# Kernel optimization log

Hardware: AMD Instinct MI355X
Metric: run time of the kernel (lower is better)

The kernel has to match this reference:

```python
import jax, jax.numpy as jnp
import numpy as np

N, E, G = 100000, 1600000, 64   # nodes, edges, graphs
IN, H, OUT = 32, 128, 3


def setup_inputs() -> dict:
    key = jax.random.key(0)
    ks = jax.random.split(key, 24)
    def w(k, i, o):
        return (jax.random.normal(k, (i, o), jnp.float32) / np.sqrt(i)).astype(jnp.float32)
    inp = {
        "x": jax.random.normal(ks[0], (N, IN), jnp.float32),
        "edge_index": jax.random.randint(ks[1], (2, E), 0, N, dtype=jnp.int32).astype(jnp.int64),
        "batch": jnp.sort(jax.random.randint(ks[2], (N,), 0, G, dtype=jnp.int32)).astype(jnp.int64),
        # SAGEConv layer 0 (in->hidden): lin_l (neighbors, with bias), lin_r (root, no bias)
        "Wl0": w(ks[3], IN, H), "bl0": jnp.zeros((H,), jnp.float32), "Wr0": w(ks[4], IN, H),
        # SAGEConv layers 1,2 (hidden->hidden)
        "Wl1": w(ks[5], H, H), "bl1": jnp.zeros((H,), jnp.float32), "Wr1": w(ks[6], H, H),
        "Wl2": w(ks[7], H, H), "bl2": jnp.zeros((H,), jnp.float32), "Wr2": w(ks[8], H, H),
        # output head
        "Wfc": w(ks[9], H, OUT), "bfc": jnp.zeros((OUT,), jnp.float32),
        # aux MLP on (dim1, dim3)
        "Wa1": w(ks[10], 2, H), "ba1": jnp.zeros((H,), jnp.float32),
        "Wa2": w(ks[11], H, H), "ba2": jnp.zeros((H,), jnp.float32),
        "Wao": w(ks[12], H, 1), "bao": jnp.zeros((1,), jnp.float32),
    }
    return inp


def _sage_conv(x, src, dst, Wl, bl, Wr):
    # PyG SAGEConv (mean aggr): out = lin_l(mean_{j in N(i)} x_j) + lin_r(x_i)
    msg = x[src]                                   # [E, d] gather
    agg = jax.ops.segment_sum(msg, dst, num_segments=N)
    cnt = jax.ops.segment_sum(jnp.ones((src.shape[0],), x.dtype), dst, num_segments=N)
    mean = agg / jnp.maximum(cnt, 1.0)[:, None]
    return mean @ Wl + bl + x @ Wr


def reference(x, edge_index, batch,
              Wl0, bl0, Wr0, Wl1, bl1, Wr1, Wl2, bl2, Wr2,
              Wfc, bfc, Wa1, ba1, Wa2, ba2, Wao, bao):
    src, dst = edge_index[0], edge_index[1]
    h = jax.nn.relu(_sage_conv(x, src, dst, Wl0, bl0, Wr0))   # dropout is identity in eval
    h = jax.nn.relu(_sage_conv(h, src, dst, Wl1, bl1, Wr1))
    h = jax.nn.relu(_sage_conv(h, src, dst, Wl2, bl2, Wr2))
    main = h @ Wfc + bfc                                      # [N, 3]
    dim1, dim3 = main[:, 0], main[:, 2]
    aux_in = jnp.stack([dim1, dim3], axis=-1)                 # [N, 2]
    a = jax.nn.relu(aux_in @ Wa1 + ba1)
    a = jax.nn.relu(a @ Wa2 + ba2)
    aux_out = (a @ Wao + bao)[:, 0]                           # [N]
    final = jnp.stack([dim1, aux_out, dim3], axis=-1)         # [N, 3]
    # global mean pool over graph ids
    s = jax.ops.segment_sum(final, batch, num_segments=G)
    c = jax.ops.segment_sum(jnp.ones((final.shape[0],), final.dtype), batch, num_segments=G)
    return s / jnp.maximum(c, 1.0)[:, None]                   # [G, 3]
```

## Files before the change

kernel.cpp:

```cpp
#include <hip/hip_runtime.h>

#define NR 128
#define PART_CH 4096
typedef unsigned short ushortT;
typedef __attribute__((ext_vector_type(8))) short short8;
typedef __attribute__((ext_vector_type(4))) float float4v;
typedef __attribute__((ext_vector_type(2))) float float2v;

__device__ __forceinline__ unsigned short f32_to_bf16_rne(float f) {
    unsigned u = __float_as_uint(f);
    unsigned r = (u + 0x7fffu + ((u >> 16) & 1u)) >> 16;
    return (unsigned short)r;
}

__device__ __forceinline__ unsigned char f32_to_fp8(float f) {
    return (unsigned char)(__builtin_amdgcn_cvt_pk_fp8_f32(f, f, 0, false) & 0xff);
}

__device__ __forceinline__ void accum8(float* acc, uint4 v) {
    unsigned u[4] = {v.x, v.y, v.z, v.w};
#pragma unroll
    for (int q = 0; q < 4; q++) {
        acc[2 * q]     += __uint_as_float(u[q] << 16);
        acc[2 * q + 1] += __uint_as_float(u[q] & 0xffff0000u);
    }
}

__device__ __forceinline__ void accum32_fp8(float* ag, uint4 A, uint4 B) {
    unsigned w[8] = {A.x, A.y, A.z, A.w, B.x, B.y, B.z, B.w};
#pragma unroll
    for (int m = 0; m < 8; m++) {
        float2v lo = __builtin_amdgcn_cvt_pk_f32_fp8(w[m], false);
        float2v hi = __builtin_amdgcn_cvt_pk_f32_fp8(w[m], true);
        ag[4 * m + 0] += lo.x;
        ag[4 * m + 1] += lo.y;
        ag[4 * m + 2] += hi.x;
        ag[4 * m + 3] += hi.y;
    }
}


__launch_bounds__(256)
__global__ void bucket_count(const int* __restrict__ dst, int* __restrict__ bcnt, int E, int NB) {
    __shared__ int h[1024];
    int t = threadIdx.x;
    for (int j = t; j < NB; j += 256) h[j] = 0;
    __syncthreads();
    int e0 = blockIdx.x * PART_CH;
    int e1 = min(e0 + PART_CH, E);
    for (int base = e0; base < e1; base += 2048) {
        int idx = base + t;
        int d[8];
        int cnt = 0;
#pragma unroll
        for (int u = 0; u < 8; u++) {
            int e = idx + u * 256;
            if (e < e1) d[cnt++] = dst[e];
        }
        for (int u = 0; u < cnt; u++) atomicAdd(&h[d[u] >> 7], 1);
    }
    __syncthreads();
    for (int j = t; j < NB; j += 256) {
        int v = h[j];
        if (v) atomicAdd(&bcnt[j], v);
    }
}

__launch_bounds__(256)
__global__ void bucket_scan(const int* __restrict__ bcnt, int* __restrict__ bstart,
                            int* __restrict__ gcur, int NB, int E) {
    __shared__ int sh[256];
    int t = threadIdx.x;
    int v[4];
    int tot = 0;
#pragma unroll
    for (int j = 0; j < 4; j++) {
        int idx = t * 4 + j;
        v[j] = (idx < NB) ? bcnt[idx] : 0;
        tot += v[j];
    }
    sh[t] = tot;
    __syncthreads();
    for (int off = 1; off < 256; off <<= 1) {
        int add = (t >= off) ? sh[t - off] : 0;
        __syncthreads();
        sh[t] += add;
        __syncthreads();
    }
    int run = sh[t] - tot;
#pragma unroll
    for (int j = 0; j < 4; j++) {
        int idx = t * 4 + j;
        if (idx < NB) { bstart[idx] = run; gcur[idx] = run; }
        run += v[j];
    }
    if (t == 0) bstart[NB] = E;
}

__launch_bounds__(256)
__global__ void partition_edges(const int* __restrict__ src, const int* __restrict__ dst,
                                int* __restrict__ gcur, unsigned* __restrict__ packed,
                                int E, int NB) {
    __shared__ int hist[1024];
    __shared__ int base[1024];
    int t = threadIdx.x;
    int e0 = blockIdx.x * PART_CH;
    int e1 = min(e0 + PART_CH, E);
    for (int j = t; j < NB; j += 256) hist[j] = 0;
    __syncthreads();
    for (int bb = e0; bb < e1; bb += 2048) {
        int idx = bb + t;
        int d[8];
        int cnt = 0;
#pragma unroll
        for (int u = 0; u < 8; u++) {
            int e = idx + u * 256;
            if (e < e1) d[cnt++] = dst[e];
        }
        for (int u = 0; u < cnt; u++) atomicAdd(&hist[d[u] >> 7], 1);
    }
    __syncthreads();
    for (int j = t; j < NB; j += 256) {
        int h = hist[j];
        base[j] = h ? atomicAdd(&gcur[j], h) : 0;
    }
    __syncthreads();
    for (int j = t; j < NB; j += 256) hist[j] = base[j];
    __syncthreads();
    for (int bb = e0; bb < e1; bb += 2048) {
        int idx = bb + t;
        int d[8], s[8];
        int cnt = 0;
#pragma unroll
        for (int u = 0; u < 8; u++) {
            int e = idx + u * 256;
            if (e < e1) { d[cnt] = dst[e]; s[cnt] = src[e]; cnt++; }
        }
        for (int u = 0; u < cnt; u++) {
            int dd = d[u];
            int pos = atomicAdd(&hist[dd >> 7], 1);
            packed[pos] = (unsigned)s[u] | ((unsigned)(dd & (NR - 1)) << 17);
        }
    }
}

__launch_bounds__(256)
__global__ void bucket_sort(const unsigned* __restrict__ packed, const int* __restrict__ bstart,
                            int* __restrict__ row_start, int* __restrict__ srcs, int N) {
    __shared__ int cnt[NR];
    __shared__ int sc[NR];
    __shared__ int cur[NR];
    int b = blockIdx.x, t = threadIdx.x;
    int nb0 = b * NR;
    int nnode = min(NR, N - nb0);
    int lo = bstart[b], hi = bstart[b + 1];
    if (t < NR) cnt[t] = 0;
    __syncthreads();
    for (int bb = lo; bb < hi; bb += 2048) {
        int idx = bb + t;
        unsigned pk[8];
        int c = 0;
#pragma unroll
        for (int u = 0; u < 8; u++) {
            int e = idx + u * 256;
            if (e < hi) pk[c++] = packed[e];
        }
        for (int u = 0; u < c; u++) atomicAdd(&cnt[pk[u] >> 17], 1);
    }
    __syncthreads();
    if (t < NR) sc[t] = cnt[t];
    __syncthreads();
    for (int off = 1; off < NR; off <<= 1) {
        int add = (t >= off && t < NR) ? sc[t - off] : 0;
        __syncthreads();
        if (t < NR) sc[t] += add;
        __syncthreads();
    }
    if (t < nnode) {
        int s = lo + sc[t] - cnt[t];
        row_start[nb0 + t] = s;
        cur[t] = s;
    }
    if (t == 0 && nb0 + nnode == N) row_start[N] = hi;
    __syncthreads();
    for (int bb = lo; bb < hi; bb += 2048) {
        int idx = bb + t;
        unsigned pk[8];
        int c = 0;
#pragma unroll
        for (int u = 0; u < 8; u++) {
            int e = idx + u * 256;
            if (e < hi) pk[c++] = packed[e];
        }
        for (int u = 0; u < c; u++) {
            int pos = atomicAdd(&cur[pk[u] >> 17], 1);
            srcs[pos] = (int)(pk[u] & 0x1FFFFu);
        }
    }
}


__global__ void prep_fused(const float* __restrict__ x, ushortT* __restrict__ xbf, int n4,
                           const float* __restrict__ Wl0, const float* __restrict__ Wr0,
                           const float* __restrict__ Wl1, const float* __restrict__ Wr1,
                           const float* __restrict__ Wl2, const float* __restrict__ Wr2,
                           const float* __restrict__ Wa2,
                           ushortT* __restrict__ Wt0, ushortT* __restrict__ Wt1,
                           ushortT* __restrict__ Wt2, ushortT* __restrict__ Wa2t) {
    int tid0 = blockIdx.x * 256 + threadIdx.x;
    if (tid0 < n4) {
        float4 v = ((const float4*)x)[tid0];
        ushort4 o;
        o.x = f32_to_bf16_rne(v.x);
        o.y = f32_to_bf16_rne(v.y);
        o.z = f32_to_bf16_rne(v.z);
        o.w = f32_to_bf16_rne(v.w);
        ((ushort4*)xbf)[tid0] = o;
        return;
    }
    int tid = tid0 - n4;
    if (tid < 8192) {
        int col = tid >> 6, k = tid & 63;
        float v = (k < 32) ? Wl0[k * 128 + col] : Wr0[(k - 32) * 128 + col];
        Wt0[col * 64 + ((k + 8 * col) & 63)] = f32_to_bf16_rne(v);
    } else if (tid < 8192 + 32768) {
        int j = tid - 8192;
        int col = j >> 8, k = j & 255;
        float v = (k < 128) ? Wl1[k * 128 + col] : Wr1[(k - 128) * 128 + col];
        Wt1[(k >> 6) * 8192 + col * 64 + (((k & 63) + 8 * col) & 63)] = f32_to_bf16_rne(v);
    } else if (tid < 8192 + 65536) {
        int j = tid - 8192 - 32768;
        int col = j >> 8, k = j & 255;
        float v = (k < 128) ? Wl2[k * 128 + col] : Wr2[(k - 128) * 128 + col];
        Wt2[(k >> 6) * 8192 + col * 64 + (((k & 63) + 8 * col) & 63)] = f32_to_bf16_rne(v);
    } else if (tid < 8192 + 65536 + 16384) {
        int j = tid - 8192 - 65536;
        int col = j >> 7, k = j & 127;
        Wa2t[(k >> 6) * 8192 + col * 64 + (((k & 63) + 8 * col) & 63)] = f32_to_bf16_rne(Wa2[k * 128 + col]);
    }
}


__device__ __forceinline__ void gather_fp8(const uint4* __restrict__ hp,
                                           const int* __restrict__ srcs,
                                           int lo, int deg, int q, float* ag) {
    if (deg <= 0) return;
    int last = lo + deg - 1;
    int nb = (deg + 1) >> 1;
    int sA0, sA1, sB0, sB1;
    uint4 A[4], B[4];
    sA0 = srcs[lo];
    sA1 = srcs[min(lo + 1, last)];
    sB0 = srcs[min(lo + 2, last)];
    sB1 = srcs[min(lo + 3, last)];
    {
        size_t b0 = (size_t)sA0 * 8 + q * 2;
        size_t b1 = (size_t)sA1 * 8 + q * 2;
        A[0] = hp[b0]; A[1] = hp[b0 + 1];
        A[2] = hp[b1]; A[3] = hp[b1 + 1];
    }
    for (int b = 0; b < nb; b++) {
        if (!(b & 1)) {
            if (b + 1 < nb) {
                size_t b0 = (size_t)sB0 * 8 + q * 2;
                size_t b1 = (size_t)sB1 * 8 + q * 2;
                B[0] = hp[b0]; B[1] = hp[b0 + 1];
                B[2] = hp[b1]; B[3] = hp[b1 + 1];
            }
            if (b + 2 < nb) {
                sA0 = srcs[min(lo + (b + 2) * 2, last)];
                sA1 = srcs[min(lo + (b + 2) * 2 + 1, last)];
            }
            int rem = deg - b * 2;
            accum32_fp8(ag, A[0], A[1]);
            if (rem > 1) accum32_fp8(ag, A[2], A[3]);
        } else {
            if (b + 1 < nb) {
                size_t b0 = (size_t)sA0 * 8 + q * 2;
                size_t b1 = (size_t)sA1 * 8 + q * 2;
                A[0] = hp[b0]; A[1] = hp[b0 + 1];
                A[2] = hp[b1]; A[3] = hp[b1 + 1];
            }
            if (b + 2 < nb) {
                sB0 = srcs[min(lo + (b + 2) * 2, last)];
                sB1 = srcs[min(lo + (b + 2) * 2 + 1, last)];
            }
            int rem = deg - b * 2;
            accum32_fp8(ag, B[0], B[1]);
            if (rem > 1) accum32_fp8(ag, B[2], B[3]);
        }
    }
}

__device__ __forceinline__ void gather_bf16(const uint4* __restrict__ xp,
                                            const int* __restrict__ srcs,
                                            int lo, int deg, int q, float* ag) {
    if (deg <= 0) return;
    int last = lo + deg - 1;
    int nb = (deg + 3) >> 2;
    int sA[4], sB[4];
    uint4 A[4], B[4];
#pragma unroll
    for (int u = 0; u < 4; u++) sA[u] = srcs[min(lo + u, last)];
#pragma unroll
    for (int u = 0; u < 4; u++) sB[u] = srcs[min(lo + 4 + u, last)];
#pragma unroll
    for (int u = 0; u < 4; u++) A[u] = xp[(size_t)sA[u] * 4 + q];
    for (int b = 0; b < nb; b++) {
        if (!(b & 1)) {
            if (b + 1 < nb) {
#pragma unroll
                for (int u = 0; u < 4; u++) B[u] = xp[(size_t)sB[u] * 4 + q];
            }
            if (b + 2 < nb) {
#pragma unroll
                for (int u = 0; u < 4; u++) sA[u] = srcs[min(lo + (b + 2) * 4 + u, last)];
            }
            int rem = deg - b * 4;
#pragma unroll
            for (int u = 0; u < 4; u++)
                if (u < rem) accum8(ag, A[u]);
        } else {
            if (b + 1 < nb) {
#pragma unroll
                for (int u = 0; u < 4; u++) A[u] = xp[(size_t)sA[u] * 4 + q];
            }
            if (b + 2 < nb) {
#pragma unroll
                for (int u = 0; u < 4; u++) sB[u] = srcs[min(lo + (b + 2) * 4 + u, last)];
            }
            int rem = deg - b * 4;
#pragma unroll
            for (int u = 0; u < 4; u++)
                if (u < rem) accum8(ag, B[u]);
        }
    }
}


__device__ __forceinline__ void stage_copy(ushortT* sW, const ushortT* Wq, int t) {
    const uint4* Wg = (const uint4*)Wq;
    uint4* Ws = (uint4*)sW;
#pragma unroll
    for (int j = 0; j < 4; j++) Ws[t + j * 256] = Wg[t + j * 256];
}

template <int KH, bool IN_FP8>
__device__ __forceinline__ void gemm_agg_body(
        const void* __restrict__ gat, const ushortT* __restrict__ Ah,
        const int* __restrict__ srcs, const int* __restrict__ rs,
        const ushortT* __restrict__ Wt, const float* __restrict__ bias,
        ushortT* __restrict__ outbf, unsigned char* __restrict__ outf8, int n) {
    constexpr int NKS = KH / 32;
    __shared__ __attribute__((aligned(16))) ushortT sW[128 * 64];
    int t = threadIdx.x;
    stage_copy(sW, Wt, t);
    int wv = t >> 6, lane = t & 63;
    int q = lane >> 4, cid = lane & 15;
    int row = blockIdx.x * 64 + wv * 16 + cid;
    int rc = min(row, n - 1);

    float ag[NKS * 8];
#pragma unroll
    for (int j = 0; j < NKS * 8; j++) ag[j] = 0.f;
    int lo = rs[rc], deg = rs[rc + 1] - lo;
    if constexpr (IN_FP8) gather_fp8((const uint4*)gat, srcs, lo, deg, q, ag);
    else                  gather_bf16((const uint4*)gat, srcs, lo, deg, q, ag);
    float inv = 1.0f / (float)max(deg, 1);
    short8 am[NKS];
#pragma unroll
    for (int ks = 0; ks < NKS; ks++)
#pragma unroll
        for (int j = 0; j < 8; j++) am[ks][j] = (short)f32_to_bf16_rne(ag[ks * 8 + j] * inv);
    short8 ah[NKS];
#pragma unroll
    for (int ks = 0; ks < NKS; ks++)
        ah[ks] = *(const short8*)(Ah + (size_t)rc * KH + ks * 32 + q * 8);
    __syncthreads();

    float4v acc[8];
#pragma unroll
    for (int j = 0; j < 8; j++) acc[j] = (float4v){0.f, 0.f, 0.f, 0.f};
    int pbase = q * 8 + 8 * cid;
    if constexpr (KH == 32) {
        {
            int p = pbase & 63;
#pragma unroll
            for (int j = 0; j < 8; ++j) {
                short8 b = *(const short8*)(sW + (j * 16 + cid) * 64 + p);
                acc[j] = __builtin_amdgcn_mfma_f32_16x16x32_bf16(am[0], b, acc[j], 0, 0, 0);
            }
        }
        {
            int p = (32 + pbase) & 63;
#pragma unroll
            for (int j = 0; j < 8; ++j) {
                short8 b = *(const short8*)(sW + (j * 16 + cid) * 64 + p);
                acc[j] = __builtin_amdgcn_mfma_f32_16x16x32_bf16(ah[0], b, acc[j], 0, 0, 0);
            }
        }
    } else {
#pragma unroll
        for (int st = 0; st < 4; st++) {
            if (st > 0) {
                __syncthreads();
                stage_copy(sW, Wt + st * 8192, t);
                __syncthreads();
            }
#pragma unroll
            for (int ksl = 0; ksl < 2; ksl++) {
                short8 a = (st < 2) ? am[st * 2 + ksl] : ah[(st - 2) * 2 + ksl];
                int p = (ksl * 32 + pbase) & 63;
#pragma unroll
                for (int j = 0; j < 8; ++j) {
                    short8 b = *(const short8*)(sW + (j * 16 + cid) * 64 + p);
                    acc[j] = __builtin_amdgcn_mfma_f32_16x16x32_bf16(a, b, acc[j], 0, 0, 0);
                }
            }
        }
    }
    float bo[8];
#pragma unroll
    for (int j = 0; j < 8; ++j) bo[j] = bias[j * 16 + cid];
    int orow = blockIdx.x * 64 + wv * 16 + q * 4;
#pragma unroll
    for (int rr = 0; rr < 4; ++rr) {
        int r = orow + rr;
        if (r < n) {
#pragma unroll
            for (int j = 0; j < 8; ++j) {
                int col = j * 16 + cid;
                float v = fmaxf(acc[j][rr] + bo[j], 0.f);
                outbf[(size_t)r * 128 + col] = f32_to_bf16_rne(v);
                int pc = ((col >> 3) & 3) * 32 + ((col >> 5) << 3) + (col & 7);
                outf8[(size_t)r * 128 + pc] = f32_to_fp8(v);
            }
        }
    }
}

__launch_bounds__(256, 2)
__global__ void gemm_agg32(const void* __restrict__ gat, const ushortT* __restrict__ Ah,
                           const int* __restrict__ srcs, const int* __restrict__ rs,
                           const ushortT* __restrict__ Wt, const float* __restrict__ bias,
                           ushortT* __restrict__ outbf, unsigned char* __restrict__ outf8, int n) {
    gemm_agg_body<32, false>(gat, Ah, srcs, rs, Wt, bias, outbf, outf8, n);
}

__launch_bounds__(256, 2)
__global__ void gemm_agg128(const void* __restrict__ gat, const ushortT* __restrict__ Ah,
                            const int* __restrict__ srcs, const int* __restrict__ rs,
                            const ushortT* __restrict__ Wt, const float* __restrict__ bias,
                            ushortT* __restrict__ outbf, unsigned char* __restrict__ outf8, int n) {
    gemm_agg_body<128, true>(gat, Ah, srcs, rs, Wt, bias, outbf, outf8, n);
}


__launch_bounds__(256, 2)
__global__ void gemm_agg_fin(const void* __restrict__ gat, const ushortT* __restrict__ Ah,
                             const int* __restrict__ srcs, const int* __restrict__ rs,
                             const ushortT* __restrict__ Wt, const float* __restrict__ bias,
                             const float* __restrict__ Wfc, const float* __restrict__ bfc,
                             const ushortT* __restrict__ Wa2t, const float* __restrict__ Wa1,
                             const float* __restrict__ ba1, const float* __restrict__ ba2,
                             const float* __restrict__ Wao, const float* __restrict__ bao,
                             float* __restrict__ fin, int n) {
    __shared__ __attribute__((aligned(16))) ushortT sW[128 * 64];
    __shared__ float sD1[64], sD3[64];
    __shared__ float sWa1a[128], sWa1b[128], sBa1[128];
    int t = threadIdx.x;
    stage_copy(sW, Wt, t);
    if (t < 128) { sWa1a[t] = Wa1[t]; sWa1b[t] = Wa1[128 + t]; sBa1[t] = ba1[t]; }
    int wv = t >> 6, lane = t & 63;
    int q = lane >> 4, cid = lane & 15;
    int row = blockIdx.x * 64 + wv * 16 + cid;
    int rc = min(row, n - 1);

    float ag[32];
#pragma unroll
    for (int j = 0; j < 32; j++) ag[j] = 0.f;
    int lo = rs[rc], deg = rs[rc + 1] - lo;
    gather_fp8((const uint4*)gat, srcs, lo, deg, q, ag);
    float inv = 1.0f / (float)max(deg, 1);
    short8 am[4];
#pragma unroll
    for (int ks = 0; ks < 4; ks++)
#pragma unroll
        for (int j = 0; j < 8; j++) am[ks][j] = (short)f32_to_bf16_rne(ag[ks * 8 + j] * inv);
    short8 ah[4];
#pragma unroll
    for (int ks = 0; ks < 4; ks++)
        ah[ks] = *(const short8*)(Ah + (size_t)rc * 128 + ks * 32 + q * 8);
    __syncthreads();

    float4v acc[8];
#pragma unroll
    for (int j = 0; j < 8; j++) acc[j] = (float4v){0.f, 0.f, 0.f, 0.f};
    int pbase = q * 8 + 8 * cid;
#pragma unroll
    for (int st = 0; st < 4; st++) {
        if (st > 0) {
            __syncthreads();
            stage_copy(sW, Wt + st * 8192, t);
            __syncthreads();
        }
#pragma unroll
        for (int ksl = 0; ksl < 2; ksl++) {
            short8 a = (st < 2) ? am[st * 2 + ksl] : ah[(st - 2) * 2 + ksl];
            int p = (ksl * 32 + pbase) & 63;
#pragma unroll
            for (int j = 0; j < 8; ++j) {
                short8 b = *(const short8*)(sW + (j * 16 + cid) * 64 + p);
                acc[j] = __builtin_amdgcn_mfma_f32_16x16x32_bf16(a, b, acc[j], 0, 0, 0);
            }
        }
    }

    float bo[8], w1[8], w3[8];
#pragma unroll
    for (int j = 0; j < 8; ++j) {
        int col = j * 16 + cid;
        bo[j] = bias[col];
        w1[j] = Wfc[col * 3 + 0];
        w3[j] = Wfc[col * 3 + 2];
    }
    float bfc0 = bfc[0], bfc2 = bfc[2];
#pragma unroll
    for (int rr = 0; rr < 4; ++rr) {
        float p1 = 0.f, p3 = 0.f;
#pragma unroll
        for (int j = 0; j < 8; ++j) {
            float v = fmaxf(acc[j][rr] + bo[j], 0.f);
            p1 += v * w1[j];
            p3 += v * w3[j];
        }
        p1 += __shfl_xor(p1, 1, 64); p3 += __shfl_xor(p3, 1, 64);
        p1 += __shfl_xor(p1, 2, 64); p3 += __shfl_xor(p3, 2, 64);
        p1 += __shfl_xor(p1, 4, 64); p3 += __shfl_xor(p3, 4, 64);
        p1 += __shfl_xor(p1, 8, 64); p3 += __shfl_xor(p3, 8, 64);
        if (cid == 0) {
            int rowl = wv * 16 + q * 4 + rr;
            float d1 = p1 + bfc0, d3 = p3 + bfc2;
            sD1[rowl] = d1;
            sD3[rowl] = d3;
            int r = blockIdx.x * 64 + rowl;
            if (r < n) {
                fin[(size_t)r * 3 + 0] = d1;
                fin[(size_t)r * 3 + 2] = d3;
            }
        }
    }
    __syncthreads();

    int rl = wv * 16 + cid;
    float d1a = sD1[rl], d3a = sD3[rl];
    float4v hacc[8];
#pragma unroll
    for (int j = 0; j < 8; j++) hacc[j] = (float4v){0.f, 0.f, 0.f, 0.f};
#pragma unroll
    for (int hs = 0; hs < 2; hs++) {
        if (hs > 0) __syncthreads();
        stage_copy(sW, Wa2t + hs * 8192, t);
        __syncthreads();
#pragma unroll
        for (int ksl = 0; ksl < 2; ++ksl) {
            int k0 = hs * 64 + ksl * 32 + q * 8;
            short8 a0;
#pragma unroll
            for (int j = 0; j < 8; ++j) {
                int k = k0 + j;
                float v0 = fmaxf(fmaf(d1a, sWa1a[k], fmaf(d3a, sWa1b[k], sBa1[k])), 0.f);
                a0[j] = (short)f32_to_bf16_rne(v0);
            }
            int p = (ksl * 32 + pbase) & 63;
#pragma unroll
            for (int j = 0; j < 8; ++j) {
                short8 b = *(const short8*)(sW + (j * 16 + cid) * 64 + p);
                hacc[j] = __builtin_amdgcn_mfma_f32_16x16x32_bf16(a0, b, hacc[j], 0, 0, 0);
            }
        }
    }
    float b2[8], wo[8];
#pragma unroll
    for (int j = 0; j < 8; ++j) {
        int col = j * 16 + cid;
        b2[j] = ba2[col];
        wo[j] = Wao[col];
    }
    float bao0 = bao[0];
#pragma unroll
    for (int rr = 0; rr < 4; ++rr) {
        float s = 0.f;
#pragma unroll
        for (int j = 0; j < 8; ++j) s += fmaxf(hacc[j][rr] + b2[j], 0.f) * wo[j];
        s += __shfl_xor(s, 1, 64);
        s += __shfl_xor(s, 2, 64);
        s += __shfl_xor(s, 4, 64);
        s += __shfl_xor(s, 8, 64);
        int r = blockIdx.x * 64 + wv * 16 + q * 4 + rr;
        if (cid == 0 && r < n) fin[(size_t)r * 3 + 1] = s + bao0;
    }
}


__global__ void pool_kernel(const float* __restrict__ fin, const int* __restrict__ batch,
                            float* __restrict__ out, int n) {
    int g = blockIdx.x, t = threadIdx.x;
    int lo = 0, hi = n;
    while (lo < hi) { int mid = (lo + hi) >> 1; if (batch[mid] < g) lo = mid + 1; else hi = mid; }
    int start = lo;
    lo = 0; hi = n;
    while (lo < hi) { int mid = (lo + hi) >> 1; if (batch[mid] < g + 1) lo = mid + 1; else hi = mid; }
    int end = lo;
    float s0 = 0.f, s1 = 0.f, s2 = 0.f;
    for (int i = start + t; i < end; i += 256) {
        s0 += fin[(size_t)i * 3 + 0];
        s1 += fin[(size_t)i * 3 + 1];
        s2 += fin[(size_t)i * 3 + 2];
    }
    __shared__ float r0[256], r1[256], r2[256];
    r0[t] = s0; r1[t] = s1; r2[t] = s2;
    __syncthreads();
    for (int off = 128; off > 0; off >>= 1) {
        if (t < off) { r0[t] += r0[t + off]; r1[t] += r1[t + off]; r2[t] += r2[t + off]; }
        __syncthreads();
    }
    if (t == 0) {
        float c = (float)max(end - start, 1);
        out[g * 3 + 0] = r0[0] / c;
        out[g * 3 + 1] = r1[0] / c;
        out[g * 3 + 2] = r2[0] / c;
    }
}


extern "C" void kernel_launch(void* const* d_in, const int* in_sizes, int n_in,
                              void* d_out, int out_size, void* d_ws, size_t ws_size,
                              hipStream_t stream) {
    const float* x    = (const float*)d_in[0];
    const int*   ei   = (const int*)d_in[1];
    const int*   batch= (const int*)d_in[2];
    const float* Wl0  = (const float*)d_in[3];
    const float* bl0  = (const float*)d_in[4];
    const float* Wr0  = (const float*)d_in[5];
    const float* Wl1  = (const float*)d_in[6];
    const float* bl1  = (const float*)d_in[7];
    const float* Wr1  = (const float*)d_in[8];
    const float* Wl2  = (const float*)d_in[9];
    const float* bl2  = (const float*)d_in[10];
    const float* Wr2  = (const float*)d_in[11];
    const float* Wfc  = (const float*)d_in[12];
    const float* bfc  = (const float*)d_in[13];
    const float* Wa1  = (const float*)d_in[14];
    const float* ba1  = (const float*)d_in[15];
    const float* Wa2  = (const float*)d_in[16];
    const float* ba2  = (const float*)d_in[17];
    const float* Wao  = (const float*)d_in[18];
    const float* bao  = (const float*)d_in[19];

    const int N = in_sizes[0] / 32;
    const int E = in_sizes[1] / 2;
    const int G = out_size / 3;
    const int* src = ei;
    const int* dst = ei + E;
    float* out = (float*)d_out;
    const int NB = (N + NR - 1) / NR;

    char* p = (char*)d_ws;
    auto carve = [&](size_t bytes) {
        void* r = (void*)p;
        p += (bytes + 255) & ~(size_t)255;
        return r;
    };
    int*           bcnt     = (int*)carve((size_t)NB * 4);
    int*           bstart   = (int*)carve((size_t)(NB + 1) * 4);
    int*           gcur     = (int*)carve((size_t)NB * 4);
    int*           row_start= (int*)carve((size_t)(N + 1) * 4);
    unsigned*      packed   = (unsigned*)carve((size_t)E * 4);
    int*           srcs     = (int*)carve((size_t)E * 4);
    ushortT*       xbf      = (ushortT*)carve((size_t)N * 32 * 2);
    ushortT*       hbf0     = (ushortT*)carve((size_t)N * 128 * 2);
    ushortT*       hbf1     = (ushortT*)carve((size_t)N * 128 * 2);
    unsigned char* hf8_0    = (unsigned char*)carve((size_t)N * 128);
    unsigned char* hf8_1    = (unsigned char*)carve((size_t)N * 128);
    float*         fin      = (float*)carve((size_t)N * 3 * 4);
    ushortT*       Wt0      = (ushortT*)carve((size_t)128 * 64 * 2);
    ushortT*       Wt1      = (ushortT*)carve((size_t)128 * 256 * 2);
    ushortT*       Wt2      = (ushortT*)carve((size_t)128 * 256 * 2);
    ushortT*       Wa2t     = (ushortT*)carve((size_t)128 * 128 * 2);

    const int gemm_grid = (N + 63) / 64;
    const int part_grid = (E + PART_CH - 1) / PART_CH;
    const int n4 = N * 32 / 4;

    prep_fused<<<(n4 + 90112 + 255) / 256, 256, 0, stream>>>(
        x, xbf, n4, Wl0, Wr0, Wl1, Wr1, Wl2, Wr2, Wa2, Wt0, Wt1, Wt2, Wa2t);

    hipMemsetAsync(bcnt, 0, (size_t)NB * 4, stream);
    bucket_count<<<part_grid, 256, 0, stream>>>(dst, bcnt, E, NB);
    bucket_scan<<<1, 256, 0, stream>>>(bcnt, bstart, gcur, NB, E);
    partition_edges<<<part_grid, 256, 0, stream>>>(src, dst, gcur, packed, E, NB);
    bucket_sort<<<NB, 256, 0, stream>>>(packed, bstart, row_start, srcs, N);

    gemm_agg32<<<gemm_grid, 256, 0, stream>>>(
        (const void*)xbf, xbf, srcs, row_start, Wt0, bl0, hbf0, hf8_0, N);
    gemm_agg128<<<gemm_grid, 256, 0, stream>>>(
        (const void*)hf8_0, hbf0, srcs, row_start, Wt1, bl1, hbf1, hf8_1, N);
    gemm_agg_fin<<<gemm_grid, 256, 0, stream>>>(
        (const void*)hf8_1, hbf1, srcs, row_start, Wt2, bl2, Wfc, bfc,
        Wa2t, Wa1, ba1, ba2, Wao, bao, fin, N);

    pool_kernel<<<G, 256, 0, stream>>>(fin, batch, out, N);
}
```

Baseline: 336.2 us.

## Split neighbor aggregation out of GEMM kernels into standalone gather kernels

Moves the mean-aggregation gather out of the fused gather+GEMM kernels into separate agg_bf16/agg_fp8 kernels. Each thread handles one 16- or 8-channel slice of a node, issues 8 independent row loads per step and writes a bf16 mean buffer. The GEMM kernels then just load the precomputed means. The aim is higher occupancy and memory-level parallelism for the gather, which no longer shares launch bounds and registers with the MFMA code. The cost is three extra launches and an extra write and read of an N×128 bf16 intermediate per layer.

```diff
diff --git a/kernel.cpp b/kernel.cpp
--- a/kernel.cpp
+++ b/kernel.cpp
@@ -26,10 +26,10 @@
     }
 }
 
-__device__ __forceinline__ void accum32_fp8(float* ag, uint4 A, uint4 B) {
-    unsigned w[8] = {A.x, A.y, A.z, A.w, B.x, B.y, B.z, B.w};
-#pragma unroll
-    for (int m = 0; m < 8; m++) {
+__device__ __forceinline__ void accum16_fp8(float* ag, uint4 v) {
+    unsigned w[4] = {v.x, v.y, v.z, v.w};
+#pragma unroll
+    for (int m = 0; m < 4; m++) {
         float2v lo = __builtin_amdgcn_cvt_pk_f32_fp8(w[m], false);
         float2v hi = __builtin_amdgcn_cvt_pk_f32_fp8(w[m], true);
         ag[4 * m + 0] += lo.x;
@@ -241,100 +241,71 @@
 }
 
 
-__device__ __forceinline__ void gather_fp8(const uint4* __restrict__ hp,
-                                           const int* __restrict__ srcs,
-                                           int lo, int deg, int q, float* ag) {
-    if (deg <= 0) return;
-    int last = lo + deg - 1;
-    int nb = (deg + 1) >> 1;
-    int sA0, sA1, sB0, sB1;
-    uint4 A[4], B[4];
-    sA0 = srcs[lo];
-    sA1 = srcs[min(lo + 1, last)];
-    sB0 = srcs[min(lo + 2, last)];
-    sB1 = srcs[min(lo + 3, last)];
-    {
-        size_t b0 = (size_t)sA0 * 8 + q * 2;
-        size_t b1 = (size_t)sA1 * 8 + q * 2;
-        A[0] = hp[b0]; A[1] = hp[b0 + 1];
-        A[2] = hp[b1]; A[3] = hp[b1 + 1];
-    }
-    for (int b = 0; b < nb; b++) {
-        if (!(b & 1)) {
-            if (b + 1 < nb) {
-                size_t b0 = (size_t)sB0 * 8 + q * 2;
-                size_t b1 = (size_t)sB1 * 8 + q * 2;
-                B[0] = hp[b0]; B[1] = hp[b0 + 1];
-                B[2] = hp[b1]; B[3] = hp[b1 + 1];
-            }
-            if (b + 2 < nb) {
-                sA0 = srcs[min(lo + (b + 2) * 2, last)];
-                sA1 = srcs[min(lo + (b + 2) * 2 + 1, last)];
-            }
-            int rem = deg - b * 2;
-            accum32_fp8(ag, A[0], A[1]);
-            if (rem > 1) accum32_fp8(ag, A[2], A[3]);
-        } else {
-            if (b + 1 < nb) {
-                size_t b0 = (size_t)sA0 * 8 + q * 2;
-                size_t b1 = (size_t)sA1 * 8 + q * 2;
-                A[0] = hp[b0]; A[1] = hp[b0 + 1];
-                A[2] = hp[b1]; A[3] = hp[b1 + 1];
-            }
-            if (b + 2 < nb) {
-                sB0 = srcs[min(lo + (b + 2) * 2, last)];
-                sB1 = srcs[min(lo + (b + 2) * 2 + 1, last)];
-            }
-            int rem = deg - b * 2;
-            accum32_fp8(ag, B[0], B[1]);
-            if (rem > 1) accum32_fp8(ag, B[2], B[3]);
-        }
-    }
-}
-
-__device__ __forceinline__ void gather_bf16(const uint4* __restrict__ xp,
-                                            const int* __restrict__ srcs,
-                                            int lo, int deg, int q, float* ag) {
-    if (deg <= 0) return;
-    int last = lo + deg - 1;
-    int nb = (deg + 3) >> 2;
-    int sA[4], sB[4];
-    uint4 A[4], B[4];
-#pragma unroll
-    for (int u = 0; u < 4; u++) sA[u] = srcs[min(lo + u, last)];
-#pragma unroll
-    for (int u = 0; u < 4; u++) sB[u] = srcs[min(lo + 4 + u, last)];
-#pragma unroll
-    for (int u = 0; u < 4; u++) A[u] = xp[(size_t)sA[u] * 4 + q];
-    for (int b = 0; b < nb; b++) {
-        if (!(b & 1)) {
-            if (b + 1 < nb) {
-#pragma unroll
-                for (int u = 0; u < 4; u++) B[u] = xp[(size_t)sB[u] * 4 + q];
-            }
-            if (b + 2 < nb) {
-#pragma unroll
-                for (int u = 0; u < 4; u++) sA[u] = srcs[min(lo + (b + 2) * 4 + u, last)];
-            }
-            int rem = deg - b * 4;
-#pragma unroll
-            for (int u = 0; u < 4; u++)
-                if (u < rem) accum8(ag, A[u]);
-        } else {
-            if (b + 1 < nb) {
-#pragma unroll
-                for (int u = 0; u < 4; u++) A[u] = xp[(size_t)sA[u] * 4 + q];
-            }
-            if (b + 2 < nb) {
-#pragma unroll
-                for (int u = 0; u < 4; u++) sB[u] = srcs[min(lo + (b + 2) * 4 + u, last)];
-            }
-            int rem = deg - b * 4;
-#pragma unroll
-            for (int u = 0; u < 4; u++)
-                if (u < rem) accum8(ag, B[u]);
-        }
-    }
+__launch_bounds__(256)
+__global__ void agg_fp8(const uint4* __restrict__ hp, const int* __restrict__ srcs,
+                        const int* __restrict__ rs, ushortT* __restrict__ amb, int n) {
+    int tid = blockIdx.x * 256 + threadIdx.x;
+    if (tid >= n * 8) return;
+    int i = tid >> 3, c = tid & 7;
+    int lo = rs[i], hi = rs[i + 1];
+    float ag[16];
+#pragma unroll
+    for (int j = 0; j < 16; j++) ag[j] = 0.f;
+    int e = lo;
+    for (; e + 8 <= hi; e += 8) {
+        int s[8];
+#pragma unroll
+        for (int u = 0; u < 8; u++) s[u] = srcs[e + u];
+        uint4 v[8];
+#pragma unroll
+        for (int u = 0; u < 8; u++) v[u] = hp[(size_t)s[u] * 8 + c];
+#pragma unroll
+        for (int u = 0; u < 8; u++) accum16_fp8(ag, v[u]);
+    }
+    for (; e < hi; ++e) accum16_fp8(ag, hp[(size_t)srcs[e] * 8 + c]);
+    float inv = 1.0f / (float)max(hi - lo, 1);
+    uint4 o0, o1;
+    o0.x = (unsigned)f32_to_bf16_rne(ag[0] * inv)  | ((unsigned)f32_to_bf16_rne(ag[1] * inv) << 16);
+    o0.y = (unsigned)f32_to_bf16_rne(ag[2] * inv)  | ((unsigned)f32_to_bf16_rne(ag[3] * inv) << 16);
+    o0.z = (unsigned)f32_to_bf16_rne(ag[4] * inv)  | ((unsigned)f32_to_bf16_rne(ag[5] * inv) << 16);
+    o0.w = (unsigned)f32_to_bf16_rne(ag[6] * inv)  | ((unsigned)f32_to_bf16_rne(ag[7] * inv) << 16);
+    o1.x = (unsigned)f32_to_bf16_rne(ag[8] * inv)  | ((unsigned)f32_to_bf16_rne(ag[9] * inv) << 16);
+    o1.y = (unsigned)f32_to_bf16_rne(ag[10] * inv) | ((unsigned)f32_to_bf16_rne(ag[11] * inv) << 16);
+    o1.z = (unsigned)f32_to_bf16_rne(ag[12] * inv) | ((unsigned)f32_to_bf16_rne(ag[13] * inv) << 16);
+    o1.w = (unsigned)f32_to_bf16_rne(ag[14] * inv) | ((unsigned)f32_to_bf16_rne(ag[15] * inv) << 16);
+    ((uint4*)amb)[(size_t)i * 16 + c * 2]     = o0;
+    ((uint4*)amb)[(size_t)i * 16 + c * 2 + 1] = o1;
+}
+
+__launch_bounds__(256)
+__global__ void agg_bf16(const uint4* __restrict__ xp, const int* __restrict__ srcs,
+                         const int* __restrict__ rs, ushortT* __restrict__ amb, int n) {
+    int tid = blockIdx.x * 256 + threadIdx.x;
+    if (tid >= n * 4) return;
+    int i = tid >> 2, c = tid & 3;
+    int lo = rs[i], hi = rs[i + 1];
+    float ag[8];
+#pragma unroll
+    for (int j = 0; j < 8; j++) ag[j] = 0.f;
+    int e = lo;
+    for (; e + 8 <= hi; e += 8) {
+        int s[8];
+#pragma unroll
+        for (int u = 0; u < 8; u++) s[u] = srcs[e + u];
+        uint4 v[8];
+#pragma unroll
+        for (int u = 0; u < 8; u++) v[u] = xp[(size_t)s[u] * 4 + c];
+#pragma unroll
+        for (int u = 0; u < 8; u++) accum8(ag, v[u]);
+    }
+    for (; e < hi; ++e) accum8(ag, xp[(size_t)srcs[e] * 4 + c]);
+    float inv = 1.0f / (float)max(hi - lo, 1);
+    uint4 o;
+    o.x = (unsigned)f32_to_bf16_rne(ag[0] * inv) | ((unsigned)f32_to_bf16_rne(ag[1] * inv) << 16);
+    o.y = (unsigned)f32_to_bf16_rne(ag[2] * inv) | ((unsigned)f32_to_bf16_rne(ag[3] * inv) << 16);
+    o.z = (unsigned)f32_to_bf16_rne(ag[4] * inv) | ((unsigned)f32_to_bf16_rne(ag[5] * inv) << 16);
+    o.w = (unsigned)f32_to_bf16_rne(ag[6] * inv) | ((unsigned)f32_to_bf16_rne(ag[7] * inv) << 16);
+    ((uint4*)amb)[(size_t)i * 4 + c] = o;
 }
 
 
@@ -345,10 +316,9 @@
     for (int j = 0; j < 4; j++) Ws[t + j * 256] = Wg[t + j * 256];
 }
 
-template <int KH, bool IN_FP8>
-__device__ __forceinline__ void gemm_agg_body(
-        const void* __restrict__ gat, const ushortT* __restrict__ Ah,
-        const int* __restrict__ srcs, const int* __restrict__ rs,
+template <int KH>
+__device__ __forceinline__ void gemm_body(
+        const ushortT* __restrict__ Amb, const ushortT* __restrict__ Ah,
         const ushortT* __restrict__ Wt, const float* __restrict__ bias,
         ushortT* __restrict__ outbf, unsigned char* __restrict__ outf8, int n) {
     constexpr int NKS = KH / 32;
@@ -360,22 +330,17 @@
     int row = blockIdx.x * 64 + wv * 16 + cid;
     int rc = min(row, n - 1);
 
-    float ag[NKS * 8];
-#pragma unroll
-    for (int j = 0; j < NKS * 8; j++) ag[j] = 0.f;
-    int lo = rs[rc], deg = rs[rc + 1] - lo;
-    if constexpr (IN_FP8) gather_fp8((const uint4*)gat, srcs, lo, deg, q, ag);
-    else                  gather_bf16((const uint4*)gat, srcs, lo, deg, q, ag);
-    float inv = 1.0f / (float)max(deg, 1);
-    short8 am[NKS];
-#pragma unroll
-    for (int ks = 0; ks < NKS; ks++)
-#pragma unroll
-        for (int j = 0; j < 8; j++) am[ks][j] = (short)f32_to_bf16_rne(ag[ks * 8 + j] * inv);
-    short8 ah[NKS];
-#pragma unroll
-    for (int ks = 0; ks < NKS; ks++)
-        ah[ks] = *(const short8*)(Ah + (size_t)rc * KH + ks * 32 + q * 8);
+    short8 am[NKS], ah[NKS];
+    if constexpr (KH == 32) {
+        am[0] = *(const short8*)(Amb + (size_t)rc * 32 + q * 8);
+        ah[0] = *(const short8*)(Ah + (size_t)rc * 32 + q * 8);
+    } else {
+#pragma unroll
+        for (int ks = 0; ks < NKS; ks++) {
+            am[ks] = *(const short8*)(Amb + (size_t)rc * 128 + q * 32 + ks * 8);
+            ah[ks] = *(const short8*)(Ah + (size_t)rc * 128 + ks * 32 + q * 8);
+        }
+    }
     __syncthreads();
 
     float4v acc[8];
@@ -440,31 +405,28 @@
 }
 
 __launch_bounds__(256, 2)
-__global__ void gemm_agg32(const void* __restrict__ gat, const ushortT* __restrict__ Ah,
-                           const int* __restrict__ srcs, const int* __restrict__ rs,
-                           const ushortT* __restrict__ Wt, const float* __restrict__ bias,
-                           ushortT* __restrict__ outbf, unsigned char* __restrict__ outf8, int n) {
-    gemm_agg_body<32, false>(gat, Ah, srcs, rs, Wt, bias, outbf, outf8, n);
+__global__ void gemm32(const ushortT* __restrict__ Amb, const ushortT* __restrict__ Ah,
+                       const ushortT* __restrict__ Wt, const float* __restrict__ bias,
+                       ushortT* __restrict__ outbf, unsigned char* __restrict__ outf8, int n) {
+    gemm_body<32>(Amb, Ah, Wt, bias, outbf, outf8, n);
 }
 
 __launch_bounds__(256, 2)
-__global__ void gemm_agg128(const void* __restrict__ gat, const ushortT* __restrict__ Ah,
-                            const int* __restrict__ srcs, const int* __restrict__ rs,
-                            const ushortT* __restrict__ Wt, const float* __restrict__ bias,
-                            ushortT* __restrict__ outbf, unsigned char* __restrict__ outf8, int n) {
-    gemm_agg_body<128, true>(gat, Ah, srcs, rs, Wt, bias, outbf, outf8, n);
+__global__ void gemm128(const ushortT* __restrict__ Amb, const ushortT* __restrict__ Ah,
+                        const ushortT* __restrict__ Wt, const float* __restrict__ bias,
+                        ushortT* __restrict__ outbf, unsigned char* __restrict__ outf8, int n) {
+    gemm_body<128>(Amb, Ah, Wt, bias, outbf, outf8, n);
 }
 
 
 __launch_bounds__(256, 2)
-__global__ void gemm_agg_fin(const void* __restrict__ gat, const ushortT* __restrict__ Ah,
-                             const int* __restrict__ srcs, const int* __restrict__ rs,
-                             const ushortT* __restrict__ Wt, const float* __restrict__ bias,
-                             const float* __restrict__ Wfc, const float* __restrict__ bfc,
-                             const ushortT* __restrict__ Wa2t, const float* __restrict__ Wa1,
-                             const float* __restrict__ ba1, const float* __restrict__ ba2,
-                             const float* __restrict__ Wao, const float* __restrict__ bao,
-                             float* __restrict__ fin, int n) {
+__global__ void gemm_fin(const ushortT* __restrict__ Amb, const ushortT* __restrict__ Ah,
+                         const ushortT* __restrict__ Wt, const float* __restrict__ bias,
+                         const float* __restrict__ Wfc, const float* __restrict__ bfc,
+                         const ushortT* __restrict__ Wa2t, const float* __restrict__ Wa1,
+                         const float* __restrict__ ba1, const float* __restrict__ ba2,
+                         const float* __restrict__ Wao, const float* __restrict__ bao,
+                         float* __restrict__ fin, int n) {
     __shared__ __attribute__((aligned(16))) ushortT sW[128 * 64];
     __shared__ float sD1[64], sD3[64];
     __shared__ float sWa1a[128], sWa1b[128], sBa1[128];
@@ -476,21 +438,12 @@
     int row = blockIdx.x * 64 + wv * 16 + cid;
     int rc = min(row, n - 1);
 
-    float ag[32];
-#pragma unroll
-    for (int j = 0; j < 32; j++) ag[j] = 0.f;
-    int lo = rs[rc], deg = rs[rc + 1] - lo;
-    gather_fp8((const uint4*)gat, srcs, lo, deg, q, ag);
-    float inv = 1.0f / (float)max(deg, 1);
-    short8 am[4];
-#pragma unroll
-    for (int ks = 0; ks < 4; ks++)
-#pragma unroll
-        for (int j = 0; j < 8; j++) am[ks][j] = (short)f32_to_bf16_rne(ag[ks * 8 + j] * inv);
-    short8 ah[4];
-#pragma unroll
-    for (int ks = 0; ks < 4; ks++)
+    short8 am[4], ah[4];
+#pragma unroll
+    for (int ks = 0; ks < 4; ks++) {
+        am[ks] = *(const short8*)(Amb + (size_t)rc * 128 + q * 32 + ks * 8);
         ah[ks] = *(const short8*)(Ah + (size_t)rc * 128 + ks * 32 + q * 8);
+    }
     __syncthreads();
 
     float4v acc[8];
@@ -683,6 +636,9 @@
     ushortT*       hbf1     = (ushortT*)carve((size_t)N * 128 * 2);
     unsigned char* hf8_0    = (unsigned char*)carve((size_t)N * 128);
     unsigned char* hf8_1    = (unsigned char*)carve((size_t)N * 128);
+    ushortT*       amb0     = (ushortT*)carve((size_t)N * 32 * 2);
+    ushortT*       amb1     = (ushortT*)carve((size_t)N * 128 * 2);
+    ushortT*       amb2     = (ushortT*)carve((size_t)N * 128 * 2);
     float*         fin      = (float*)carve((size_t)N * 3 * 4);
     ushortT*       Wt0      = (ushortT*)carve((size_t)128 * 64 * 2);
     ushortT*       Wt1      = (ushortT*)carve((size_t)128 * 256 * 2);
@@ -702,13 +658,16 @@
     partition_edges<<<part_grid, 256, 0, stream>>>(src, dst, gcur, packed, E, NB);
     bucket_sort<<<NB, 256, 0, stream>>>(packed, bstart, row_start, srcs, N);
 
-    gemm_agg32<<<gemm_grid, 256, 0, stream>>>(
-        (const void*)xbf, xbf, srcs, row_start, Wt0, bl0, hbf0, hf8_0, N);
-    gemm_agg128<<<gemm_grid, 256, 0, stream>>>(
-        (const void*)hf8_0, hbf0, srcs, row_start, Wt1, bl1, hbf1, hf8_1, N);
-    gemm_agg_fin<<<gemm_grid, 256, 0, stream>>>(
-        (const void*)hf8_1, hbf1, srcs, row_start, Wt2, bl2, Wfc, bfc,
-        Wa2t, Wa1, ba1, ba2, Wao, bao, fin, N);
+    agg_bf16<<<(N * 4 + 255) / 256, 256, 0, stream>>>(
+        (const uint4*)xbf, srcs, row_start, amb0, N);
+    gemm32<<<gemm_grid, 256, 0, stream>>>(amb0, xbf, Wt0, bl0, hbf0, hf8_0, N);
+    agg_fp8<<<(N * 8 + 255) / 256, 256, 0, stream>>>(
+        (const uint4*)hf8_0, srcs, row_start, amb1, N);
+    gemm128<<<gemm_grid, 256, 0, stream>>>(amb1, hbf0, Wt1, bl1, hbf1, hf8_1, N);
+    agg_fp8<<<(N * 8 + 255) / 256, 256, 0, stream>>>(
+        (const uint4*)hf8_1, srcs, row_start, amb2, N);
+    gemm_fin<<<gemm_grid, 256, 0, stream>>>(
+        amb2, hbf1, Wt2, bl2, Wfc, bfc, Wa2t, Wa1, ba1, ba2, Wao, bao, fin, N);
 
     pool_kernel<<<G, 256, 0, stream>>>(fin, batch, out, N);
 }
```

Result: slower. 354.5 us (+5.4%).
